# Kernel tuning notes

Hardware: AMD Instinct MI355X
Metric: run time of the kernel (lower is better)

The kernel has to match this reference:

```python
import jax, jax.numpy as jnp
import numpy as np

B, N, D, H = 2, 2048, 1024, 16
DH = D // H  # 64


def setup_inputs() -> dict:
    key = jax.random.key(0)
    k1, k2, k3, k4, k5 = jax.random.split(key, 5)
    x = jax.random.normal(k1, (B, N, D), dtype=jnp.float32)
    # per-head kqv Linear weights, stacked: [H, D, 3*DH] (acts as x @ W)
    W_kqv = jax.random.normal(k2, (H, D, 3 * DH), dtype=jnp.float32) * 0.02
    b_kqv = jax.random.normal(k3, (H, 3 * DH), dtype=jnp.float32) * 0.02
    W_proj = jax.random.normal(k4, (D, D), dtype=jnp.float32) * 0.02
    b_proj = jax.random.normal(k5, (D,), dtype=jnp.float32) * 0.02
    return {"x": x, "W_kqv": W_kqv, "b_kqv": b_kqv, "W_proj": W_proj, "b_proj": b_proj}


def reference(x, W_kqv, b_kqv, W_proj, b_proj):
    # per-head projections, all heads batched: [B, H, N, 3*DH]
    kqv = jnp.einsum('bnd,hde->bhne', x, W_kqv) + b_kqv[None, :, None, :]
    # original chunk order is k, q, v
    k, q, v = jnp.split(kqv, 3, axis=-1)  # each [B, H, N, DH]
    # scores: A = q @ k^T / sqrt(DH)  -> [B, H, N, N]
    A = jnp.einsum('bhnd,bhmd->bhnm', q, k) / jnp.sqrt(jnp.asarray(DH, x.dtype))
    causal = jnp.tril(jnp.ones((N, N), dtype=bool))
    A = jnp.where(causal[None, None, :, :], A, -jnp.inf)
    attn = jax.nn.softmax(A, axis=-1)
    sa = jnp.einsum('bhnm,bhmd->bhnd', attn, v)          # [B, H, N, DH]
    sa = sa.transpose(0, 2, 1, 3).reshape(B, N, D)        # concat heads
    out = sa @ W_proj.T + b_proj                          # output projection
    return out
```

## Files before the change

kernel.cpp:

```cpp
#include <hip/hip_runtime.h>
#include <hip/hip_bf16.h>
#include <cstdint>
#include <cstddef>

#define B_  2
#define N_  2048
#define D_  1024
#define H_  16
#define DH_ 64
#define E3_ 192

typedef __attribute__((ext_vector_type(8))) short short8;
typedef __attribute__((ext_vector_type(8))) unsigned short ushort8v;
typedef __attribute__((ext_vector_type(4))) float floatx4;

static __device__ __forceinline__ unsigned short f2bf(float f) {
  union { float f; unsigned u; } c; c.f = f;
  unsigned r = c.u + 0x7fffu + ((c.u >> 16) & 1u);
  return (unsigned short)(r >> 16);
}

#define MFMA(a,b,c) __builtin_amdgcn_mfma_f32_16x16x32_bf16((a),(b),(c),0,0,0)

#define GL_LDS16(g, l) __builtin_amdgcn_global_load_lds( \
    (const __attribute__((address_space(1))) void*)(g),  \
    (__attribute__((address_space(3))) void*)(l), 16, 0, 0)

__global__ __launch_bounds__(256) void k_prep(const float* __restrict__ x,
                                              const float* __restrict__ Wkqv,
                                              const float* __restrict__ Wproj,
                                              unsigned short* __restrict__ Xb,
                                              unsigned short* __restrict__ Wt,
                                              unsigned short* __restrict__ Wpb) {
  __shared__ float tile[64][65];
  int bx = blockIdx.x, t = threadIdx.x;
  if (bx < 2048 || bx >= 2816) {
    const float* in = (bx < 2048) ? x : Wproj;
    unsigned short* out = (bx < 2048) ? Xb : Wpb;
    int i = ((bx < 2048) ? bx : bx - 2816) * 256 + t;
    const float4* p = (const float4*)in + (size_t)i * 2;
    float4 a = p[0], b = p[1];
    ushort8v o;
    o[0]=f2bf(a.x); o[1]=f2bf(a.y); o[2]=f2bf(a.z); o[3]=f2bf(a.w);
    o[4]=f2bf(b.x); o[5]=f2bf(b.y); o[6]=f2bf(b.z); o[7]=f2bf(b.w);
    *((ushort8v*)out + i) = o;
    return;
  }
  int idx = bx - 2048;
  int d0 = (idx & 15) * 64, rem = idx >> 4;
  int cat = rem % 3, h = rem / 3, e0 = cat * 64;
  const float* Wp = Wkqv + (size_t)h * D_ * E3_;
  int dr = t >> 2, ec = (t & 3) * 16;
#pragma unroll
  for (int j = 0; j < 16; j += 4) {
    float4 wv = *(const float4*)&Wp[(size_t)(d0 + dr) * E3_ + e0 + ec + j];
    tile[dr][ec + j + 0] = wv.x; tile[dr][ec + j + 1] = wv.y;
    tile[dr][ec + j + 2] = wv.z; tile[dr][ec + j + 3] = wv.w;
  }
  __syncthreads();
  int er = t >> 2, dc = (t & 3) * 16;
  ushort8v o0, o1;
#pragma unroll
  for (int j = 0; j < 8; j++) o0[j] = f2bf(tile[dc + j][er]);
#pragma unroll
  for (int j = 0; j < 8; j++) o1[j] = f2bf(tile[dc + 8 + j][er]);
  size_t o = ((size_t)(cat * 1024 + h * 64 + er)) * D_ + d0 + dc;
  *(ushort8v*)&Wt[o]     = o0;
  *(ushort8v*)&Wt[o + 8] = o1;
}

__global__ __launch_bounds__(512, 2) void k_qkv(const unsigned short* __restrict__ Xb,
                                                const unsigned short* __restrict__ Wt,
                                                const float* __restrict__ bkqv,
                                                unsigned short* __restrict__ Qb,
                                                unsigned short* __restrict__ Kb,
                                                unsigned short* __restrict__ Vt) {
  __shared__ unsigned short LDSf[65536];
  const int t = threadIdx.x;
  const int wid = t >> 6, lane = t & 63, quad = lane >> 4, l16 = lane & 15;
  const int wr = wid >> 2, wc = wid & 3;
  const int m0 = blockIdx.x * 256, c0 = blockIdx.y * 256;

  floatx4 acc[8][4];
#pragma unroll
  for (int i = 0; i < 8; i++)
#pragma unroll
    for (int j = 0; j < 4; j++) acc[i][j] = (floatx4){0.f, 0.f, 0.f, 0.f};

  const int slr = t >> 3;
  const int sco = ((t & 7) ^ (slr & 7)) * 8;
  const unsigned short* gA0 = Xb + (size_t)(m0 +   0 + slr) * D_ + sco;
  const unsigned short* gA1 = Xb + (size_t)(m0 +  64 + slr) * D_ + sco;
  const unsigned short* gA2 = Xb + (size_t)(m0 + 128 + slr) * D_ + sco;
  const unsigned short* gA3 = Xb + (size_t)(m0 + 192 + slr) * D_ + sco;
  const unsigned short* gB0 = Wt + (size_t)(c0 +   0 + slr) * D_ + sco;
  const unsigned short* gB1 = Wt + (size_t)(c0 +  64 + slr) * D_ + sco;
  const unsigned short* gB2 = Wt + (size_t)(c0 + 128 + slr) * D_ + sco;
  const unsigned short* gB3 = Wt + (size_t)(c0 + 192 + slr) * D_ + sco;
#define SA(gp, q, s, bb) GL_LDS16((gp) + (s) * 64, &LDSf[(bb) * 16384 + (q) * 4096 + t * 8])
#define SB(gp, q, s, bb) GL_LDS16((gp) + (s) * 64, &LDSf[32768 + (bb) * 16384 + (q) * 4096 + t * 8])

  const int aoff0 = ((quad)     ^ (l16 & 7)) * 8;
  const int aoff1 = ((4 + quad) ^ (l16 & 7)) * 8;
  const unsigned short* Abase = &LDSf[(wr * 128 + l16) * 64];
  const unsigned short* Bbase = &LDSf[32768 + (wc * 64 + l16) * 64];

  SA(gA0, 0, 0, 0); SA(gA1, 1, 0, 0); SA(gA2, 2, 0, 0); SA(gA3, 3, 0, 0);
  SB(gB0, 0, 0, 0); SB(gB1, 1, 0, 0); SB(gB2, 2, 0, 0); SB(gB3, 3, 0, 0);
  SA(gA0, 0, 1, 1); SA(gA2, 2, 1, 1);
  asm volatile("s_waitcnt vmcnt(2)" ::: "memory");
  __builtin_amdgcn_s_barrier();

  for (int s = 0; s < 16; s++) {
    const int buf = s & 1, nbuf = buf ^ 1;
    const int so = buf * 16384;
    short8 a[4][2], b[4][2];
#pragma unroll
    for (int mi = 0; mi < 4; mi++) {
      a[mi][0] = *(const short8*)&Abase[so + mi * 1024 + aoff0];
      a[mi][1] = *(const short8*)&Abase[so + mi * 1024 + aoff1];
    }
#pragma unroll
    for (int ni = 0; ni < 2; ni++) {
      b[ni][0] = *(const short8*)&Bbase[so + ni * 1024 + aoff0];
      b[ni][1] = *(const short8*)&Bbase[so + ni * 1024 + aoff1];
    }
    if (s < 15) {
      SA(gA1, 1, s + 1, nbuf); SA(gA3, 3, s + 1, nbuf);
      SB(gB0, 0, s + 1, nbuf); SB(gB1, 1, s + 1, nbuf);
      SB(gB2, 2, s + 1, nbuf); SB(gB3, 3, s + 1, nbuf);
    }
    __builtin_amdgcn_s_barrier();
    asm volatile("s_waitcnt lgkmcnt(0)" ::: "memory");
    __builtin_amdgcn_sched_barrier(0);
    __builtin_amdgcn_s_setprio(1);
#pragma unroll
    for (int mi = 0; mi < 4; mi++)
#pragma unroll
      for (int ni = 0; ni < 2; ni++) {
        acc[mi][ni] = MFMA(a[mi][0], b[ni][0], acc[mi][ni]);
        acc[mi][ni] = MFMA(a[mi][1], b[ni][1], acc[mi][ni]);
      }
    __builtin_amdgcn_s_setprio(0);
    __builtin_amdgcn_s_barrier();
#pragma unroll
    for (int ni = 2; ni < 4; ni++) {
      b[ni][0] = *(const short8*)&Bbase[so + ni * 1024 + aoff0];
      b[ni][1] = *(const short8*)&Bbase[so + ni * 1024 + aoff1];
    }
    __builtin_amdgcn_s_barrier();
    asm volatile("s_waitcnt lgkmcnt(0)" ::: "memory");
    __builtin_amdgcn_sched_barrier(0);
    __builtin_amdgcn_s_setprio(1);
#pragma unroll
    for (int mi = 0; mi < 4; mi++)
#pragma unroll
      for (int ni = 2; ni < 4; ni++) {
        acc[mi][ni] = MFMA(a[mi][0], b[ni][0], acc[mi][ni]);
        acc[mi][ni] = MFMA(a[mi][1], b[ni][1], acc[mi][ni]);
      }
    __builtin_amdgcn_s_setprio(0);
    __builtin_amdgcn_s_barrier();
#pragma unroll
    for (int mi = 0; mi < 4; mi++) {
      a[mi][0] = *(const short8*)&Abase[so + (mi + 4) * 1024 + aoff0];
      a[mi][1] = *(const short8*)&Abase[so + (mi + 4) * 1024 + aoff1];
    }
    if (s < 14) { SA(gA0, 0, s + 2, buf); SA(gA2, 2, s + 2, buf); }
    __builtin_amdgcn_s_barrier();
    asm volatile("s_waitcnt lgkmcnt(0)" ::: "memory");
    __builtin_amdgcn_sched_barrier(0);
    __builtin_amdgcn_s_setprio(1);
#pragma unroll
    for (int mi = 0; mi < 4; mi++)
#pragma unroll
      for (int ni = 0; ni < 2; ni++) {
        acc[mi + 4][ni] = MFMA(a[mi][0], b[ni][0], acc[mi + 4][ni]);
        acc[mi + 4][ni] = MFMA(a[mi][1], b[ni][1], acc[mi + 4][ni]);
      }
    __builtin_amdgcn_s_setprio(0);
    __builtin_amdgcn_s_barrier();
    __builtin_amdgcn_s_setprio(1);
#pragma unroll
    for (int mi = 0; mi < 4; mi++)
#pragma unroll
      for (int ni = 2; ni < 4; ni++) {
        acc[mi + 4][ni] = MFMA(a[mi][0], b[ni][0], acc[mi + 4][ni]);
        acc[mi + 4][ni] = MFMA(a[mi][1], b[ni][1], acc[mi + 4][ni]);
      }
    __builtin_amdgcn_s_setprio(0);
    if (s < 14) { asm volatile("s_waitcnt vmcnt(2)" ::: "memory"); }
    else        { asm volatile("s_waitcnt vmcnt(0)" ::: "memory"); }
    __builtin_amdgcn_s_barrier();
  }

  __syncthreads();
  unsigned short* scr = &LDSf[wid * 8192];
  const int cat = c0 >> 10;
  const int h   = ((c0 + wc * 64) >> 6) & 15;
  const int bb  = (m0 + wr * 128) >> 11;
  const int n0b = (m0 + wr * 128) & (N_ - 1);
  const int l8 = lane & 7, lh = lane >> 3;
  if (cat < 2) {
    const float scale = (cat == 1) ? 0.125f : 1.0f;
    float bias[4];
#pragma unroll
    for (int ni = 0; ni < 4; ni++) bias[ni] = bkqv[h * E3_ + cat * 64 + ni * 16 + l16];
#pragma unroll
    for (int mi = 0; mi < 8; mi++)
#pragma unroll
      for (int ni = 0; ni < 4; ni++)
#pragma unroll
        for (int r = 0; r < 4; r++) {
          int rl = mi * 16 + quad * 4 + r, cl = ni * 16 + l16;
          scr[rl * 64 + ((((cl >> 3) ^ rl) & 7) * 8) + (cl & 7)] =
              f2bf((acc[mi][ni][r] + bias[ni]) * scale);
        }
    asm volatile("s_waitcnt lgkmcnt(0)" ::: "memory");
    unsigned short* dst = (cat == 0) ? Kb : Qb;
#pragma unroll
    for (int j = 0; j < 16; j++) {
      int rl = j * 8 + lh;
      short8 vv = *(const short8*)&scr[rl * 64 + ((l8 ^ lh) * 8)];
      *(short8*)&dst[((size_t)(bb * H_ + h) * N_ + n0b + rl) * DH_ + l8 * 8] = vv;
    }
  } else {
    float bias[4];
#pragma unroll
    for (int ni = 0; ni < 4; ni++) bias[ni] = bkqv[h * E3_ + 128 + ni * 16 + l16];
#pragma unroll
    for (int mi = 0; mi < 8; mi++)
#pragma unroll
      for (int ni = 0; ni < 4; ni++)
#pragma unroll
        for (int r = 0; r < 4; r++) {
          int nl = mi * 16 + quad * 4 + r, e = ni * 16 + l16;
          scr[e * 128 + ((((nl >> 3) ^ e) & 15) * 8) + (nl & 7)] =
              f2bf(acc[mi][ni][r] + bias[ni]);
        }
    asm volatile("s_waitcnt lgkmcnt(0)" ::: "memory");
#pragma unroll
    for (int j = 0; j < 16; j++) {
      int e = (j & 7) * 8 + lh;
      int nc = l8 + (j >> 3) * 8;
      short8 vv = *(const short8*)&scr[e * 128 + (((nc ^ e) & 15) * 8)];
      *(short8*)&Vt[((size_t)(bb * H_ + h) * DH_ + e) * N_ + n0b + nc * 8] = vv;
    }
  }
#undef SA
#undef SB
}

__global__ __launch_bounds__(256) void k_flash(const unsigned short* __restrict__ Qb,
                                               const unsigned short* __restrict__ Kb,
                                               const unsigned short* __restrict__ Vt,
                                               unsigned short* __restrict__ sab) {
  int bh = blockIdx.x;
  int yr = blockIdx.y, g = yr >> 3, o = yr & 7;
  int qb = (g == 0) ? o : (g == 1) ? 31 - o : (g == 2) ? 8 + o : 23 - o;
  int q0b = qb * 64;
  int wave = threadIdx.x >> 6;
  int lane = threadIdx.x & 63, quad = lane >> 4, l16 = lane & 15;
  const unsigned short* Qp = Qb + (size_t)bh * N_ * DH_;
  const unsigned short* Kp = Kb + (size_t)bh * N_ * DH_;
  const unsigned short* Vp = Vt + (size_t)bh * DH_ * N_;
  __shared__ unsigned short Klds[2][2 * 64 * 32];
  __shared__ unsigned short Vlds[2][2 * 64 * 32];
  __shared__ unsigned short Plds[4][16 * 64];
  unsigned short* P = Plds[wave];

  int q0w = q0b + wave * 16;
  short8 qf0 = *(const short8*)&Qp[(q0w + l16) * DH_ + quad * 8];
  short8 qf1 = *(const short8*)&Qp[(q0w + l16) * DH_ + 32 + quad * 8];

  int swz = ((lane & 3) ^ ((lane >> 3) & 3)) * 8;
  const unsigned short* gK = Kp + (size_t)(wave * 16 + (lane >> 2)) * DH_ + swz;
  const unsigned short* gV = Vp + (size_t)(wave * 16 + (lane >> 2)) * N_ + swz;
  int lofs = (wave * 16) * 32;
  int xr = ((l16 >> 1) & 3) * 8;
  int pxr = l16 & 7;

  floatx4 O[4];
  float lr[4];
#pragma unroll
  for (int r = 0; r < 4; r++) { O[r] = (floatx4){0.f, 0.f, 0.f, 0.f}; lr[r] = 0.f; }

  int nt = (q0b >> 6) + 1;
  GL_LDS16(gK,      &Klds[0][lofs]);
  GL_LDS16(gK + 32, &Klds[0][lofs + 64 * 32]);
  GL_LDS16(gV,      &Vlds[0][lofs]);
  GL_LDS16(gV + 32, &Vlds[0][lofs + 64 * 32]);

  for (int i = 0; i < nt; i++) {
    int buf = i & 1;
    __syncthreads();
    if (i + 1 < nt) {
      int kvn = (i + 1) << 6;
      GL_LDS16(gK + (size_t)kvn * DH_,      &Klds[buf ^ 1][lofs]);
      GL_LDS16(gK + (size_t)kvn * DH_ + 32, &Klds[buf ^ 1][lofs + 64 * 32]);
      GL_LDS16(gV + kvn,                    &Vlds[buf ^ 1][lofs]);
      GL_LDS16(gV + kvn + 32,               &Vlds[buf ^ 1][lofs + 64 * 32]);
    }
    short8 kf[4][2], vf[4][2];
#pragma unroll
    for (int c = 0; c < 4; c++) {
      kf[c][0] = *(const short8*)&Klds[buf][(c * 16 + l16) * 32 + ((quad * 8) ^ xr)];
      kf[c][1] = *(const short8*)&Klds[buf][(64 + c * 16 + l16) * 32 + ((quad * 8) ^ xr)];
      vf[c][0] = *(const short8*)&Vlds[buf][(c * 16 + l16) * 32 + ((quad * 8) ^ xr)];
      vf[c][1] = *(const short8*)&Vlds[buf][(64 + c * 16 + l16) * 32 + ((quad * 8) ^ xr)];
    }
    floatx4 s[4];
#pragma unroll
    for (int c = 0; c < 4; c++) {
      s[c] = (floatx4){0.f, 0.f, 0.f, 0.f};
      s[c] = MFMA(qf0, kf[c][0], s[c]);
      s[c] = MFMA(qf1, kf[c][1], s[c]);
    }
    if (i == nt - 1) {
#pragma unroll
      for (int c = 0; c < 4; c++)
#pragma unroll
        for (int r = 0; r < 4; r++) {
          int row = wave * 16 + quad * 4 + r;
          if (c * 16 + l16 > row) s[c][r] = -1e30f;
        }
    }
#pragma unroll
    for (int c = 0; c < 4; c++)
#pragma unroll
      for (int r = 0; r < 4; r++)
        s[c][r] = __builtin_amdgcn_exp2f(s[c][r] * 1.44269504f);
#pragma unroll
    for (int r = 0; r < 4; r++)
      lr[r] += (s[0][r] + s[1][r]) + (s[2][r] + s[3][r]);
#pragma unroll
    for (int c = 0; c < 4; c++) {
      int ch = c * 2 + (l16 >> 3);
#pragma unroll
      for (int r = 0; r < 4; r++) {
        int row = quad * 4 + r;
        P[row * 64 + ((ch ^ (row & 7)) * 8) + (l16 & 7)] = f2bf(s[c][r]);
      }
    }
    __asm__ volatile("s_waitcnt lgkmcnt(0)" ::: "memory");
    short8 pa0 = *(const short8*)&P[l16 * 64 + ((quad ^ pxr) * 8)];
    short8 pa1 = *(const short8*)&P[l16 * 64 + (((quad + 4) ^ pxr) * 8)];
    __asm__ volatile("" ::: "memory");
#pragma unroll
    for (int dt = 0; dt < 4; dt++) {
      O[dt] = MFMA(pa0, vf[dt][0], O[dt]);
      O[dt] = MFMA(pa1, vf[dt][1], O[dt]);
    }
  }
#pragma unroll
  for (int m = 1; m < 16; m <<= 1)
#pragma unroll
    for (int r = 0; r < 4; r++) lr[r] += __shfl_xor(lr[r], m);

  int b = bh >> 4, h = bh & 15;
#pragma unroll
  for (int r = 0; r < 4; r++) {
    float inv = 1.0f / lr[r];
    size_t base = ((size_t)b * N_ + q0w + quad * 4 + r) * D_ + h * DH_;
#pragma unroll
    for (int dt = 0; dt < 4; dt++) sab[base + dt * 16 + l16] = f2bf(O[dt][r] * inv);
  }
}

__global__ __launch_bounds__(256) void k_proj(const unsigned short* __restrict__ sab,
                                              const unsigned short* __restrict__ Wpb,
                                              const float* __restrict__ bproj,
                                              float* __restrict__ out) {
  __shared__ unsigned short Alds[2][2][64 * 32];
  __shared__ unsigned short Blds[2][2][64 * 32];
  int t = threadIdx.x;
  int m0 = blockIdx.x * 64, c0 = blockIdx.y * 64;
  int wave = t >> 6, lane = t & 63, quad = lane >> 4, l16 = lane & 15;
  int wm = (wave >> 1) * 32, wn = (wave & 1) * 32;
  floatx4 acc[2][2];
#pragma unroll
  for (int i = 0; i < 2; i++) { acc[i][0] = (floatx4){0,0,0,0}; acc[i][1] = (floatx4){0,0,0,0}; }

  int swz = ((lane & 3) ^ ((lane >> 3) & 3)) * 8;
  const unsigned short* gA = sab + (size_t)(m0 + wave * 16 + (lane >> 2)) * D_ + swz;
  const unsigned short* gB = Wpb + (size_t)(c0 + wave * 16 + (lane >> 2)) * D_ + swz;
  int lofs = (wave * 16) * 32;
  int xr = ((l16 >> 1) & 3) * 8;

  GL_LDS16(gA,      &Alds[0][0][lofs]);
  GL_LDS16(gA + 32, &Alds[0][1][lofs]);
  GL_LDS16(gB,      &Blds[0][0][lofs]);
  GL_LDS16(gB + 32, &Blds[0][1][lofs]);

  for (int i = 0; i < 16; i++) {
    int buf = i & 1;
    __syncthreads();
    if (i + 1 < 16) {
      int k0 = (i + 1) * 64;
      GL_LDS16(gA + k0,      &Alds[buf ^ 1][0][lofs]);
      GL_LDS16(gA + k0 + 32, &Alds[buf ^ 1][1][lofs]);
      GL_LDS16(gB + k0,      &Blds[buf ^ 1][0][lofs]);
      GL_LDS16(gB + k0 + 32, &Blds[buf ^ 1][1][lofs]);
    }
#pragma unroll
    for (int kk = 0; kk < 2; kk++) {
      short8 a[2], b[2];
#pragma unroll
      for (int mi = 0; mi < 2; mi++) a[mi] = *(const short8*)&Alds[buf][kk][(wm + mi * 16 + l16) * 32 + ((quad * 8) ^ xr)];
#pragma unroll
      for (int ni = 0; ni < 2; ni++) b[ni] = *(const short8*)&Blds[buf][kk][(wn + ni * 16 + l16) * 32 + ((quad * 8) ^ xr)];
#pragma unroll
      for (int mi = 0; mi < 2; mi++)
#pragma unroll
        for (int ni = 0; ni < 2; ni++) acc[mi][ni] = MFMA(a[mi], b[ni], acc[mi][ni]);
    }
  }
#pragma unroll
  for (int mi = 0; mi < 2; mi++)
#pragma unroll
    for (int ni = 0; ni < 2; ni++) {
      int col = c0 + wn + ni * 16 + l16;
      int grow = m0 + wm + mi * 16 + quad * 4;
      float bias = bproj[col];
#pragma unroll
      for (int r = 0; r < 4; r++)
        out[(size_t)(grow + r) * D_ + col] = acc[mi][ni][r] + bias;
    }
}

extern "C" void kernel_launch(void* const* d_in, const int* in_sizes, int n_in,
                              void* d_out, int out_size, void* d_ws, size_t ws_size,
                              hipStream_t stream) {
  const float* x     = (const float*)d_in[0];
  const float* Wkqv  = (const float*)d_in[1];
  const float* bkqv  = (const float*)d_in[2];
  const float* Wproj = (const float*)d_in[3];
  const float* bproj = (const float*)d_in[4];
  float* out = (float*)d_out;

  char* w = (char*)d_ws;
  unsigned short* Xb  = (unsigned short*)(w);
  unsigned short* Wt  = (unsigned short*)(w + (8u  << 20));
  unsigned short* Wpb = (unsigned short*)(w + (14u << 20));
  unsigned short* Qb  = (unsigned short*)(w + (16u << 20));
  unsigned short* Kb  = (unsigned short*)(w + (24u << 20));
  unsigned short* Vt  = (unsigned short*)(w + (32u << 20));
  unsigned short* sa  = (unsigned short*)(w + (40u << 20));

  k_prep<<<2048 + 768 + 512, 256, 0, stream>>>(x, Wkqv, Wproj, Xb, Wt, Wpb);
  k_qkv<<<dim3(B_ * N_ / 256, 3072 / 256), 512, 0, stream>>>(Xb, Wt, bkqv, Qb, Kb, Vt);
  k_flash<<<dim3(B_ * H_, N_ / 64), 256, 0, stream>>>(Qb, Kb, Vt, sa);
  k_proj<<<dim3(B_ * N_ / 64, D_ / 64), 256, 0, stream>>>(sa, Wpb, bproj, out);
}
```

Measured before the change: 179.1 us.

## Restructure flash kernel into paired causal query tiles with two-wave blocks

```diff
diff --git a/kernel.cpp b/kernel.cpp
--- a/kernel.cpp
+++ b/kernel.cpp
@@ -202,7 +202,7 @@
   const int n0b = (m0 + wr * 128) & (N_ - 1);
   const int l8 = lane & 7, lh = lane >> 3;
   if (cat < 2) {
-    const float scale = (cat == 1) ? 0.125f : 1.0f;
+    const float scale = (cat == 1) ? 0.18033688011112042f : 1.0f;
     float bias[4];
 #pragma unroll
     for (int ni = 0; ni < 4; ni++) bias[ni] = bkqv[h * E3_ + cat * 64 + ni * 16 + l16];
@@ -251,119 +251,123 @@
 #undef SB
 }
 
-__global__ __launch_bounds__(256) void k_flash(const unsigned short* __restrict__ Qb,
+__global__ __launch_bounds__(128) void k_flash(const unsigned short* __restrict__ Qb,
                                                const unsigned short* __restrict__ Kb,
                                                const unsigned short* __restrict__ Vt,
                                                unsigned short* __restrict__ sab) {
-  int bh = blockIdx.x;
-  int yr = blockIdx.y, g = yr >> 3, o = yr & 7;
-  int qb = (g == 0) ? o : (g == 1) ? 31 - o : (g == 2) ? 8 + o : 23 - o;
-  int q0b = qb * 64;
-  int wave = threadIdx.x >> 6;
-  int lane = threadIdx.x & 63, quad = lane >> 4, l16 = lane & 15;
+  const int bh = blockIdx.x, pr = blockIdx.y;
+  const int t = threadIdx.x;
+  const int wave = t >> 6, lane = t & 63, quad = lane >> 4, l16 = lane & 15;
   const unsigned short* Qp = Qb + (size_t)bh * N_ * DH_;
   const unsigned short* Kp = Kb + (size_t)bh * N_ * DH_;
   const unsigned short* Vp = Vt + (size_t)bh * DH_ * N_;
-  __shared__ unsigned short Klds[2][2 * 64 * 32];
-  __shared__ unsigned short Vlds[2][2 * 64 * 32];
-  __shared__ unsigned short Plds[4][16 * 64];
+  __shared__ unsigned short Klds[2][4096];
+  __shared__ unsigned short Vlds[2][4096];
+  __shared__ unsigned short Plds[2][1024];
   unsigned short* P = Plds[wave];
 
-  int q0w = q0b + wave * 16;
-  short8 qf0 = *(const short8*)&Qp[(q0w + l16) * DH_ + quad * 8];
-  short8 qf1 = *(const short8*)&Qp[(q0w + l16) * DH_ + 32 + quad * 8];
-
-  int swz = ((lane & 3) ^ ((lane >> 3) & 3)) * 8;
-  const unsigned short* gK = Kp + (size_t)(wave * 16 + (lane >> 2)) * DH_ + swz;
-  const unsigned short* gV = Vp + (size_t)(wave * 16 + (lane >> 2)) * N_ + swz;
-  int lofs = (wave * 16) * 32;
-  int xr = ((l16 >> 1) & 3) * 8;
-  int pxr = l16 & 7;
-
-  floatx4 O[4];
-  float lr[4];
-#pragma unroll
-  for (int r = 0; r < 4; r++) { O[r] = (floatx4){0.f, 0.f, 0.f, 0.f}; lr[r] = 0.f; }
-
-  int nt = (q0b >> 6) + 1;
-  GL_LDS16(gK,      &Klds[0][lofs]);
-  GL_LDS16(gK + 32, &Klds[0][lofs + 64 * 32]);
-  GL_LDS16(gV,      &Vlds[0][lofs]);
-  GL_LDS16(gV + 32, &Vlds[0][lofs + 64 * 32]);
-
-  for (int i = 0; i < nt; i++) {
-    int buf = i & 1;
+  const int srow = t >> 3;
+  const int sco = ((t & 7) ^ (srow & 7)) * 8;
+  const unsigned short* gK = Kp + (size_t)srow * DH_ + sco;
+  const unsigned short* gV = Vp + (size_t)srow * N_ + sco;
+  const int ldst = t * 8;
+  const int xr = l16 & 7;
+  const int b = bh >> 4, h = bh & 15;
+
+  for (int hf = 0; hf < 2; hf++) {
+    const int q32 = hf ? (63 - pr) : pr;
+    const int q0w = q32 * 32 + wave * 16;
+    short8 qf0 = *(const short8*)&Qp[(q0w + l16) * DH_ + quad * 8];
+    short8 qf1 = *(const short8*)&Qp[(q0w + l16) * DH_ + 32 + quad * 8];
+    floatx4 O[4];
+    float lr[4];
+#pragma unroll
+    for (int r = 0; r < 4; r++) { O[r] = (floatx4){0.f, 0.f, 0.f, 0.f}; lr[r] = 0.f; }
+    const int nt = (q32 >> 1) + 1;
+
     __syncthreads();
-    if (i + 1 < nt) {
-      int kvn = (i + 1) << 6;
-      GL_LDS16(gK + (size_t)kvn * DH_,      &Klds[buf ^ 1][lofs]);
-      GL_LDS16(gK + (size_t)kvn * DH_ + 32, &Klds[buf ^ 1][lofs + 64 * 32]);
-      GL_LDS16(gV + kvn,                    &Vlds[buf ^ 1][lofs]);
-      GL_LDS16(gV + kvn + 32,               &Vlds[buf ^ 1][lofs + 64 * 32]);
-    }
-    short8 kf[4][2], vf[4][2];
-#pragma unroll
-    for (int c = 0; c < 4; c++) {
-      kf[c][0] = *(const short8*)&Klds[buf][(c * 16 + l16) * 32 + ((quad * 8) ^ xr)];
-      kf[c][1] = *(const short8*)&Klds[buf][(64 + c * 16 + l16) * 32 + ((quad * 8) ^ xr)];
-      vf[c][0] = *(const short8*)&Vlds[buf][(c * 16 + l16) * 32 + ((quad * 8) ^ xr)];
-      vf[c][1] = *(const short8*)&Vlds[buf][(64 + c * 16 + l16) * 32 + ((quad * 8) ^ xr)];
-    }
-    floatx4 s[4];
-#pragma unroll
-    for (int c = 0; c < 4; c++) {
-      s[c] = (floatx4){0.f, 0.f, 0.f, 0.f};
-      s[c] = MFMA(qf0, kf[c][0], s[c]);
-      s[c] = MFMA(qf1, kf[c][1], s[c]);
-    }
-    if (i == nt - 1) {
+#pragma unroll
+    for (int j = 0; j < 4; j++) {
+      GL_LDS16(gK + (size_t)(j * 16) * DH_, &Klds[0][j * 1024 + ldst]);
+      GL_LDS16(gV + (size_t)(j * 16) * N_,  &Vlds[0][j * 1024 + ldst]);
+    }
+
+    for (int i = 0; i < nt; i++) {
+      const int buf = i & 1;
+      __syncthreads();
+      if (i + 1 < nt) {
+        size_t ko = (size_t)(i + 1) * 64 * DH_;
+        int vo = (i + 1) * 64;
+#pragma unroll
+        for (int j = 0; j < 4; j++) {
+          GL_LDS16(gK + ko + (size_t)(j * 16) * DH_, &Klds[buf ^ 1][j * 1024 + ldst]);
+          GL_LDS16(gV + vo + (size_t)(j * 16) * N_,  &Vlds[buf ^ 1][j * 1024 + ldst]);
+        }
+      }
+      short8 kf[4][2], vf[4][2];
+#pragma unroll
+      for (int c = 0; c < 4; c++) {
+        int rk = (c * 16 + l16) * 64;
+        kf[c][0] = *(const short8*)&Klds[buf][rk + ((quad ^ xr) * 8)];
+        kf[c][1] = *(const short8*)&Klds[buf][rk + (((quad + 4) ^ xr) * 8)];
+        vf[c][0] = *(const short8*)&Vlds[buf][rk + ((quad ^ xr) * 8)];
+        vf[c][1] = *(const short8*)&Vlds[buf][rk + (((quad + 4) ^ xr) * 8)];
+      }
+      floatx4 s[4];
+#pragma unroll
+      for (int c = 0; c < 4; c++) {
+        s[c] = (floatx4){0.f, 0.f, 0.f, 0.f};
+        s[c] = MFMA(qf0, kf[c][0], s[c]);
+        s[c] = MFMA(qf1, kf[c][1], s[c]);
+      }
+      if (i == nt - 1) {
+#pragma unroll
+        for (int c = 0; c < 4; c++)
+#pragma unroll
+          for (int r = 0; r < 4; r++) {
+            int keyg = i * 64 + c * 16 + l16;
+            int rowg = q0w + quad * 4 + r;
+            if (keyg > rowg) s[c][r] = -1e30f;
+          }
+      }
 #pragma unroll
       for (int c = 0; c < 4; c++)
 #pragma unroll
+        for (int r = 0; r < 4; r++)
+          s[c][r] = __builtin_amdgcn_exp2f(s[c][r]);
+#pragma unroll
+      for (int r = 0; r < 4; r++)
+        lr[r] += (s[0][r] + s[1][r]) + (s[2][r] + s[3][r]);
+#pragma unroll
+      for (int c = 0; c < 4; c++) {
+        int ch = c * 2 + (l16 >> 3);
+#pragma unroll
         for (int r = 0; r < 4; r++) {
-          int row = wave * 16 + quad * 4 + r;
-          if (c * 16 + l16 > row) s[c][r] = -1e30f;
+          int row = quad * 4 + r;
+          P[row * 64 + ((ch ^ (row & 7)) * 8) + (l16 & 7)] = f2bf(s[c][r]);
         }
-    }
-#pragma unroll
-    for (int c = 0; c < 4; c++)
-#pragma unroll
-      for (int r = 0; r < 4; r++)
-        s[c][r] = __builtin_amdgcn_exp2f(s[c][r] * 1.44269504f);
-#pragma unroll
-    for (int r = 0; r < 4; r++)
-      lr[r] += (s[0][r] + s[1][r]) + (s[2][r] + s[3][r]);
-#pragma unroll
-    for (int c = 0; c < 4; c++) {
-      int ch = c * 2 + (l16 >> 3);
-#pragma unroll
-      for (int r = 0; r < 4; r++) {
-        int row = quad * 4 + r;
-        P[row * 64 + ((ch ^ (row & 7)) * 8) + (l16 & 7)] = f2bf(s[c][r]);
-      }
-    }
-    __asm__ volatile("s_waitcnt lgkmcnt(0)" ::: "memory");
-    short8 pa0 = *(const short8*)&P[l16 * 64 + ((quad ^ pxr) * 8)];
-    short8 pa1 = *(const short8*)&P[l16 * 64 + (((quad + 4) ^ pxr) * 8)];
-    __asm__ volatile("" ::: "memory");
-#pragma unroll
-    for (int dt = 0; dt < 4; dt++) {
-      O[dt] = MFMA(pa0, vf[dt][0], O[dt]);
-      O[dt] = MFMA(pa1, vf[dt][1], O[dt]);
-    }
-  }
-#pragma unroll
-  for (int m = 1; m < 16; m <<= 1)
-#pragma unroll
-    for (int r = 0; r < 4; r++) lr[r] += __shfl_xor(lr[r], m);
-
-  int b = bh >> 4, h = bh & 15;
-#pragma unroll
-  for (int r = 0; r < 4; r++) {
-    float inv = 1.0f / lr[r];
-    size_t base = ((size_t)b * N_ + q0w + quad * 4 + r) * D_ + h * DH_;
-#pragma unroll
-    for (int dt = 0; dt < 4; dt++) sab[base + dt * 16 + l16] = f2bf(O[dt][r] * inv);
+      }
+      __asm__ volatile("s_waitcnt lgkmcnt(0)" ::: "memory");
+      short8 pa0 = *(const short8*)&P[l16 * 64 + ((quad ^ xr) * 8)];
+      short8 pa1 = *(const short8*)&P[l16 * 64 + (((quad + 4) ^ xr) * 8)];
+      __asm__ volatile("" ::: "memory");
+#pragma unroll
+      for (int dt = 0; dt < 4; dt++) {
+        O[dt] = MFMA(pa0, vf[dt][0], O[dt]);
+        O[dt] = MFMA(pa1, vf[dt][1], O[dt]);
+      }
+    }
+#pragma unroll
+    for (int m = 1; m < 16; m <<= 1)
+#pragma unroll
+      for (int r = 0; r < 4; r++) lr[r] += __shfl_xor(lr[r], m);
+#pragma unroll
+    for (int r = 0; r < 4; r++) {
+      float inv = 1.0f / lr[r];
+      size_t base = ((size_t)b * N_ + q0w + quad * 4 + r) * D_ + h * DH_;
+#pragma unroll
+      for (int dt = 0; dt < 4; dt++) sab[base + dt * 16 + l16] = f2bf(O[dt][r] * inv);
+    }
   }
 }
 
@@ -449,6 +453,6 @@
 
   k_prep<<<2048 + 768 + 512, 256, 0, stream>>>(x, Wkqv, Wproj, Xb, Wt, Wpb);
   k_qkv<<<dim3(B_ * N_ / 256, 3072 / 256), 512, 0, stream>>>(Xb, Wt, bkqv, Qb, Kb, Vt);
-  k_flash<<<dim3(B_ * H_, N_ / 64), 256, 0, stream>>>(Qb, Kb, Vt, sa);
+  k_flash<<<dim3(B_ * H_, 32), 128, 0, stream>>>(Qb, Kb, Vt, sa);
   k_proj<<<dim3(B_ * N_ / 64, D_ / 64), 256, 0, stream>>>(sa, Wpb, bproj, out);
 }
```

Measured after the change: 180.3 us. Within noise of the previous version (+0.7%).

## Prefetch K/V two tiles ahead in attention and fold log2e into Q scale

Applied to the files above, without the earlier changes.

```diff
diff --git a/kernel.cpp b/kernel.cpp
--- a/kernel.cpp
+++ b/kernel.cpp
@@ -202,7 +202,7 @@
   const int n0b = (m0 + wr * 128) & (N_ - 1);
   const int l8 = lane & 7, lh = lane >> 3;
   if (cat < 2) {
-    const float scale = (cat == 1) ? 0.125f : 1.0f;
+    const float scale = (cat == 1) ? 0.18033688011112042f : 1.0f;
     float bias[4];
 #pragma unroll
     for (int ni = 0; ni < 4; ni++) bias[ni] = bkqv[h * E3_ + cat * 64 + ni * 16 + l16];
@@ -280,27 +280,29 @@
   int xr = ((l16 >> 1) & 3) * 8;
   int pxr = l16 & 7;
 
+#define FSTAGE(ii, bb) do {                                              \
+    size_t ko_ = (size_t)(ii) * 64 * DH_; int vo_ = (ii) * 64;           \
+    GL_LDS16(gK + ko_,      &Klds[bb][lofs]);                            \
+    GL_LDS16(gK + ko_ + 32, &Klds[bb][lofs + 64 * 32]);                  \
+    GL_LDS16(gV + vo_,      &Vlds[bb][lofs]);                            \
+    GL_LDS16(gV + vo_ + 32, &Vlds[bb][lofs + 64 * 32]);                  \
+  } while (0)
+
   floatx4 O[4];
   float lr[4];
 #pragma unroll
   for (int r = 0; r < 4; r++) { O[r] = (floatx4){0.f, 0.f, 0.f, 0.f}; lr[r] = 0.f; }
 
   int nt = (q0b >> 6) + 1;
-  GL_LDS16(gK,      &Klds[0][lofs]);
-  GL_LDS16(gK + 32, &Klds[0][lofs + 64 * 32]);
-  GL_LDS16(gV,      &Vlds[0][lofs]);
-  GL_LDS16(gV + 32, &Vlds[0][lofs + 64 * 32]);
+  FSTAGE(0, 0);
+  if (nt > 1) FSTAGE(1, 1);
 
   for (int i = 0; i < nt; i++) {
     int buf = i & 1;
-    __syncthreads();
-    if (i + 1 < nt) {
-      int kvn = (i + 1) << 6;
-      GL_LDS16(gK + (size_t)kvn * DH_,      &Klds[buf ^ 1][lofs]);
-      GL_LDS16(gK + (size_t)kvn * DH_ + 32, &Klds[buf ^ 1][lofs + 64 * 32]);
-      GL_LDS16(gV + kvn,                    &Vlds[buf ^ 1][lofs]);
-      GL_LDS16(gV + kvn + 32,               &Vlds[buf ^ 1][lofs + 64 * 32]);
-    }
+    if (i + 1 < nt) { asm volatile("s_waitcnt vmcnt(4)" ::: "memory"); }
+    else            { asm volatile("s_waitcnt vmcnt(0)" ::: "memory"); }
+    __builtin_amdgcn_s_barrier();
+    __builtin_amdgcn_sched_barrier(0);
     short8 kf[4][2], vf[4][2];
 #pragma unroll
     for (int c = 0; c < 4; c++) {
@@ -329,7 +331,7 @@
     for (int c = 0; c < 4; c++)
 #pragma unroll
       for (int r = 0; r < 4; r++)
-        s[c][r] = __builtin_amdgcn_exp2f(s[c][r] * 1.44269504f);
+        s[c][r] = __builtin_amdgcn_exp2f(s[c][r]);
 #pragma unroll
     for (int r = 0; r < 4; r++)
       lr[r] += (s[0][r] + s[1][r]) + (s[2][r] + s[3][r]);
@@ -351,7 +353,12 @@
       O[dt] = MFMA(pa0, vf[dt][0], O[dt]);
       O[dt] = MFMA(pa1, vf[dt][1], O[dt]);
     }
-  }
+    __builtin_amdgcn_s_barrier();
+    __builtin_amdgcn_sched_barrier(0);
+    if (i + 2 < nt) FSTAGE(i + 2, buf);
+  }
+#undef FSTAGE
+
 #pragma unroll
   for (int m = 1; m < 16; m <<= 1)
 #pragma unroll
```

Measured after the change: 172.5 us. 1.04x faster.
